# Optimization experiments

Hardware: AMD Instinct MI355X
Metric: run time of the kernel (lower is better)

## Reference

```python
import jax, jax.numpy as jnp
import numpy as np

B, C, N, S, DCONV = 16, 128, 2000, 8, 4
DI = 2 * N            # mamba expand=2
DT_RANK = (N + 15) // 16


def setup_inputs() -> dict:
    key = jax.random.key(0)
    ks = jax.random.split(key, 10)
    r = lambda k, sh, s=0.02: jax.random.normal(k, sh, jnp.float32) * s
    return {
        "x": jax.random.normal(ks[0], (B, C, N, 1), jnp.float32),
        "bn1_g": jnp.ones((C,), jnp.float32), "bn1_b": jnp.zeros((C,), jnp.float32),
        "conv1_w": r(ks[1], (C, C)), "conv1_b": jnp.zeros((C,), jnp.float32),
        "ln_w": jnp.ones((N,), jnp.float32), "ln_b": jnp.zeros((N,), jnp.float32),
        "W_in": r(ks[2], (2 * DI, N)),
        "convm_w": r(ks[3], (DI, DCONV), 0.1), "convm_b": jnp.zeros((DI,), jnp.float32),
        "W_x": r(ks[4], (DT_RANK + 2 * S, DI)),
        "W_dt": r(ks[5], (DI, DT_RANK), 0.1), "b_dt": jnp.full((DI,), -2.0, jnp.float32),
        "A_log": jnp.log(jnp.broadcast_to(jnp.arange(1, S + 1, dtype=jnp.float32), (DI, S))),
        "D_p": jnp.ones((DI,), jnp.float32),
        "W_out": r(ks[6], (N, DI)),
        "bn3_g": jnp.ones((C,), jnp.float32), "bn3_b": jnp.zeros((C,), jnp.float32),
        "conv3_w": r(ks[7], (C, C)), "conv3_b": jnp.zeros((C,), jnp.float32),
    }


def _inorm(x, eps=1e-3):
    # InstanceNorm2d (no affine): per-sample, per-channel over spatial dims
    m = x.mean(axis=(2, 3), keepdims=True)
    v = x.var(axis=(2, 3), keepdims=True)
    return (x - m) * jax.lax.rsqrt(v + eps)


def _bnorm(x, g, b, eps=1e-5):
    # BatchNorm2d (training-mode stats) over (B, H, W) per channel
    m = x.mean(axis=(0, 2, 3), keepdims=True)
    v = x.var(axis=(0, 2, 3), keepdims=True)
    return (x - m) * jax.lax.rsqrt(v + eps) * g[None, :, None, None] + b[None, :, None, None]


def _block(x, g, b, w, cb):
    # InstanceNorm -> BatchNorm -> ReLU -> 1x1 Conv2d
    h = jax.nn.relu(_bnorm(_inorm(x), g, b))
    return jnp.einsum('bcnw,oc->bonw', h, w) + cb[None, :, None, None]


def _mamba(u, W_in, cw, cb, W_x, W_dt, b_dt, A_log, D_p, W_out):
    # u: [B, L, D] with L=C (seq), D=N (d_model)
    L = u.shape[1]
    xz = jnp.einsum('bld,ed->ble', u, W_in)          # [B,L,2*DI]
    xi, z = jnp.split(xz, 2, axis=-1)
    # depthwise causal conv1d along L (d_conv=4)
    xp = jnp.pad(xi, ((0, 0), (DCONV - 1, 0), (0, 0)))
    xc = sum(xp[:, k:k + L, :] * cw[:, k] for k in range(DCONV)) + cb
    xc = jax.nn.silu(xc)                             # [B,L,DI]
    xdbl = jnp.einsum('bld,ed->ble', xc, W_x)        # [B,L,dt_rank+2S]
    dt = jax.nn.softplus(jnp.einsum('blr,dr->bld', xdbl[..., :DT_RANK], W_dt) + b_dt)
    Bm = xdbl[..., DT_RANK:DT_RANK + S]              # [B,L,S]
    Cm = xdbl[..., DT_RANK + S:]                     # [B,L,S]
    A = -jnp.exp(A_log)                              # [DI,S]

    def step(h, inp):
        dt_l, B_l, C_l, u_l = inp                    # [B,DI],[B,S],[B,S],[B,DI]
        dA = jnp.exp(dt_l[..., None] * A)            # [B,DI,S]
        h = dA * h + (dt_l * u_l)[..., None] * B_l[:, None, :]
        return h, jnp.einsum('bds,bs->bd', h, C_l)

    seq = (jnp.swapaxes(dt, 0, 1), jnp.swapaxes(Bm, 0, 1),
           jnp.swapaxes(Cm, 0, 1), jnp.swapaxes(xc, 0, 1))
    h0 = jnp.zeros((u.shape[0], DI, S), u.dtype)
    _, ys = jax.lax.scan(step, h0, seq)              # ys: [L,B,DI]
    y = jnp.swapaxes(ys, 0, 1) + xc * D_p
    y = y * jax.nn.silu(z)
    return jnp.einsum('ble,de->bld', y, W_out)       # [B,L,D]


def reference(x, bn1_g, bn1_b, conv1_w, conv1_b, ln_w, ln_b, W_in, convm_w,
              convm_b, W_x, W_dt, b_dt, A_log, D_p, W_out, bn3_g, bn3_b,
              conv3_w, conv3_b):
    out = _block(x, bn1_g, bn1_b, conv1_w, conv1_b)[..., 0]   # [B,C,N]
    mu = out.mean(-1, keepdims=True)
    var = out.var(-1, keepdims=True)
    out_n = (out - mu) * jax.lax.rsqrt(var + 1e-5) * ln_w + ln_b  # LayerNorm(points)
    out = out + _mamba(out_n, W_in, convm_w, convm_b, W_x, W_dt, b_dt, A_log, D_p, W_out)
    out = _block(out[..., None], bn3_g, bn3_b, conv3_w, conv3_b)  # [B,C,N,1]
    return out + x
```

## Files before the change

### kernel.cpp

```cpp
#include <hip/hip_runtime.h>
#include <cmath>
#include <cstdint>

#define Bc   16
#define Cc   128
#define Nc   2000
#define Lc   128
#define DIc  4000
#define Sc   8
#define RKc  125
#define E2c  8000
#define EXc  141

#define KP1  2016
#define NP1  8064

__device__ __forceinline__ unsigned short f2bf(float f) {
  union { float f; unsigned int u; } v; v.f = f;
  unsigned int r = v.u + 0x7FFFu + ((v.u >> 16) & 1u);
  return (unsigned short)(r >> 16);
}

__global__ void inorm_stats(const float* __restrict__ in,
                            float* __restrict__ mout,
                            float* __restrict__ vout) {
  int bc = blockIdx.x;
  const float* p = in + (long)bc * Nc;
  float s = 0.f, sq = 0.f;
  for (int i = threadIdx.x; i < Nc; i += blockDim.x) {
    float x = p[i]; s += x; sq += x * x;
  }
  #pragma unroll
  for (int o = 32; o > 0; o >>= 1) {
    s  += __shfl_down(s, o, 64);
    sq += __shfl_down(sq, o, 64);
  }
  __shared__ float ss[4], sqq[4];
  int w = threadIdx.x >> 6, lane = threadIdx.x & 63;
  if (lane == 0) { ss[w] = s; sqq[w] = sq; }
  __syncthreads();
  if (threadIdx.x == 0) {
    s  = ss[0] + ss[1] + ss[2] + ss[3];
    sq = sqq[0] + sqq[1] + sqq[2] + sqq[3];
    float mean = s / Nc;
    float var  = sq / Nc - mean * mean;
    mout[bc] = mean; vout[bc] = var;
  }
}

__global__ void bn_scale(const float* __restrict__ v, float* __restrict__ bnsc) {
  int c = threadIdx.x;
  if (c >= Cc) return;
  float s = 0.f;
  for (int b = 0; b < Bc; b++) {
    float vv = v[b * Cc + c];
    s += vv / (vv + 1e-3f);
  }
  bnsc[c] = rsqrtf(s / Bc + 1e-5f);
}

__global__ void compute_h_t(const float* __restrict__ in,
                            const float* __restrict__ m,
                            const float* __restrict__ v,
                            const float* __restrict__ bnsc,
                            const float* __restrict__ g,
                            const float* __restrict__ bb,
                            unsigned short* __restrict__ hT) {
  int b  = blockIdx.y;
  int n0 = blockIdx.x * 64;
  __shared__ unsigned short tile[64][132];
  int t  = threadIdx.x;
  int nl = t & 63, cb = t >> 6;
  int n  = n0 + nl;
  #pragma unroll 4
  for (int p = 0; p < 32; p++) {
    int c = p * 4 + cb;
    float val = 0.f;
    if (n < Nc) {
      int bc = b * Cc + c;
      float xn = (in[(long)bc * Nc + n] - m[bc]) * rsqrtf(v[bc] + 1e-3f);
      val = fmaxf(xn * bnsc[c] * g[c] + bb[c], 0.f);
    }
    tile[nl][c] = f2bf(val);
  }
  __syncthreads();
  int r = t >> 2, c0 = (t & 3) * 32;
  int nr = n0 + r;
  if (nr < Nc) {
    unsigned int* dst = (unsigned int*)(hT + ((long)b * 2048 + nr) * 128 + c0);
    const unsigned short* src = &tile[r][c0];
    #pragma unroll
    for (int j = 0; j < 16; j++)
      dst[j] = *(const unsigned int*)(src + 2 * j);
  }
}

__global__ void reduce_slices(const float* __restrict__ sl, float* __restrict__ dst,
                              long stride, int ns, int total, int accum) {
  int i = blockIdx.x * 256 + threadIdx.x;
  if (i >= total) return;
  float s = accum ? dst[i] : 0.f;
  for (int k = 0; k < ns; k++) s += sl[(long)k * stride + i];
  dst[i] = s;
}

__global__ void reduce_xdbl(const float* __restrict__ sl,
                            float* __restrict__ xd,
                            unsigned short* __restrict__ xdb) {
  int i = blockIdx.x * 256 + threadIdx.x;
  if (i >= 2048 * 144) return;
  int row = i / 144, c = i - row * 144;
  float s = 0.f;
  if (c < EXc) {
    #pragma unroll
    for (int k = 0; k < 4; k++) s += sl[(long)k * (2048 * 256) + (long)row * 256 + c];
    xd[(long)row * EXc + c] = s;
  }
  if (c < 128) xdb[(long)row * 128 + c] = f2bf(c < RKc ? s : 0.f);
}

__global__ void cvt_pad_bf16(const float* __restrict__ src, unsigned short* __restrict__ dst,
                             int R, int Cdst, int Rsrc, int Csrc) {
  long i = (long)blockIdx.x * 256 + threadIdx.x;
  long total = (long)R * Cdst;
  if (i >= total) return;
  int r = (int)(i / Cdst), c = (int)(i - (long)r * Cdst);
  float v = (r < Rsrc && c < Csrc) ? src[(long)r * Csrc + c] : 0.f;
  dst[i] = f2bf(v);
}

__global__ void ln_rows(const float* __restrict__ in,
                        const float* __restrict__ lw,
                        const float* __restrict__ lb,
                        unsigned short* __restrict__ An) {
  int row = blockIdx.x;
  const float* p = in + (long)row * Nc;
  float s = 0.f, sq = 0.f;
  for (int i = threadIdx.x; i < Nc; i += blockDim.x) {
    float x = p[i]; s += x; sq += x * x;
  }
  #pragma unroll
  for (int o = 32; o > 0; o >>= 1) {
    s  += __shfl_down(s, o, 64);
    sq += __shfl_down(sq, o, 64);
  }
  __shared__ float ss[4], sqq[4];
  __shared__ float smean, srstd;
  int w = threadIdx.x >> 6, lane = threadIdx.x & 63;
  if (lane == 0) { ss[w] = s; sqq[w] = sq; }
  __syncthreads();
  if (threadIdx.x == 0) {
    s  = ss[0] + ss[1] + ss[2] + ss[3];
    sq = sqq[0] + sqq[1] + sqq[2] + sqq[3];
    float mean = s / Nc;
    float var  = sq / Nc - mean * mean;
    smean = mean; srstd = rsqrtf(var + 1e-5f);
  }
  __syncthreads();
  float mu = smean, rs = srstd;
  for (int i = threadIdx.x; i < KP1; i += blockDim.x) {
    float v = 0.f;
    if (i < Nc) v = (p[i] - mu) * rs * lw[i] + lb[i];
    An[(long)row * KP1 + i] = f2bf(v);
  }
}

typedef short v8s __attribute__((ext_vector_type(8)));
typedef float v4f __attribute__((ext_vector_type(4)));

typedef const __attribute__((address_space(1))) unsigned int* as1_cu32p;
typedef __attribute__((address_space(3))) unsigned int* as3_u32p;

__device__ __forceinline__ void gload_lds16(const unsigned short* g, unsigned short* l) {
  __builtin_amdgcn_global_load_lds((as1_cu32p)(uintptr_t)g,
                                   (as3_u32p)(uintptr_t)l, 16, 0, 0);
}

__global__ __launch_bounds__(256, 4)
void gemm_mfma_bt(const unsigned short* __restrict__ A,
                  const unsigned short* __restrict__ B,
                  float* C, int NN, int K, int lda, int ldb, int ldc,
                  long sA, long sB, long sC,
                  int KS, int Klen, long sliceStride,
                  int epi, const float* __restrict__ ebias,
                  const float* __restrict__ addp) {
  __shared__ unsigned short As[128 * 32];
  __shared__ unsigned short Bs[128 * 32];

  int z = blockIdx.z;
  int batch = z / KS, ks = z - batch * KS;
  const unsigned short* Ab = A + (long)batch * sA;
  const unsigned short* Bb = B + (long)batch * sB;
  float* Cs = C + (long)batch * sC + (long)ks * sliceStride;
  const float* X = addp ? addp + (long)batch * sC : nullptr;

  int k0 = ks * Klen;
  int kend = min(K, k0 + Klen);

  int i0 = blockIdx.y * 128;
  int j0 = blockIdx.x * 128;

  int t = threadIdx.x;
  int wave = t >> 6, lane = t & 63;
  int wm = wave >> 1, wn = wave & 1;

  int srow = lane >> 2;
  int scol = lane & 3;
  const unsigned short* gA0 = Ab + (long)(i0 + wave * 32 + srow) * lda + scol * 8;
  const unsigned short* gA1 = gA0 + (long)16 * lda;
  const unsigned short* gB0 = Bb + (long)(j0 + wave * 32 + srow) * ldb + scol * 8;
  const unsigned short* gB1 = gB0 + (long)16 * ldb;
  unsigned short* lA0 = As + (wave * 32) * 32;
  unsigned short* lA1 = As + (wave * 32 + 16) * 32;
  unsigned short* lB0 = Bs + (wave * 32) * 32;
  unsigned short* lB1 = Bs + (wave * 32 + 16) * 32;

  int fr = lane & 15;
  int kq = lane >> 4;

  v4f acc[4][4] = {};

  for (int kt = k0; kt < kend; kt += 32) {
    gload_lds16(gA0 + kt, lA0);
    gload_lds16(gA1 + kt, lA1);
    gload_lds16(gB0 + kt, lB0);
    gload_lds16(gB1 + kt, lB1);
    __syncthreads();

    v8s af[4], bfr[4];
    #pragma unroll
    for (int mt = 0; mt < 4; mt++)
      af[mt] = *(const v8s*)&As[(wm * 64 + mt * 16 + fr) * 32 + kq * 8];
    #pragma unroll
    for (int nt = 0; nt < 4; nt++)
      bfr[nt] = *(const v8s*)&Bs[(wn * 64 + nt * 16 + fr) * 32 + kq * 8];

    #pragma unroll
    for (int mt = 0; mt < 4; mt++)
      #pragma unroll
      for (int nt = 0; nt < 4; nt++)
        acc[mt][nt] = __builtin_amdgcn_mfma_f32_16x16x32_bf16(
            af[mt], bfr[nt], acc[mt][nt], 0, 0, 0);
    __syncthreads();
  }

  int orow = (lane >> 4) * 4;
  int ocol = lane & 15;
  #pragma unroll
  for (int mt = 0; mt < 4; mt++) {
    #pragma unroll
    for (int nt = 0; nt < 4; nt++) {
      int gi = i0 + wm * 64 + mt * 16 + orow;
      int gj = j0 + wn * 64 + nt * 16 + ocol;
      if (gj >= NN) continue;
      #pragma unroll
      for (int r = 0; r < 4; r++) {
        long idx = (long)(gi + r) * ldc + gj;
        float v = acc[mt][nt][r];
        if (epi == 1) {
          float tr = v + ebias[gj];
          v = fmaxf(tr, 0.f) + log1pf(__expf(-fabsf(tr)));
        } else if (epi == 2) {
          if (gj >= DIc) v = v / (1.f + __expf(-v));
        } else if (epi == 3) {
          v += ebias[gi + r];
          if (X) v += X[idx];
        }
        Cs[idx] = v;
      }
    }
  }
}

__global__ void dwconv_silu(const float* __restrict__ xz,
                            const float4* __restrict__ cw,
                            const float* __restrict__ cb,
                            float* __restrict__ xc,
                            unsigned short* __restrict__ xcb, int total) {
  int i = blockIdx.x * 256 + threadIdx.x;
  if (i >= total) return;
  int d  = i % DIc;
  int bl = i / DIc;
  int l  = bl % Lc;
  int b  = bl / Lc;
  float4 w = cw[d];
  float acc = cb[d];
  long rowbase = (long)(b * Lc) * E2c + d;
  int l0 = l - 3;
  if (l0     >= 0) acc += xz[rowbase + (long)l0       * E2c] * w.x;
  if (l0 + 1 >= 0) acc += xz[rowbase + (long)(l0 + 1) * E2c] * w.y;
  if (l0 + 2 >= 0) acc += xz[rowbase + (long)(l0 + 2) * E2c] * w.z;
  acc += xz[rowbase + (long)l * E2c] * w.w;
  float sv = acc / (1.f + __expf(-acc));
  xc[i] = sv;
  xcb[i] = f2bf(sv);
}

#define SCU 4
__global__ __launch_bounds__(256)
void scan_kernel(const float* __restrict__ dtv,
                 const float* __restrict__ xdbl,
                 const float* __restrict__ xc,
                 const float* __restrict__ xzf,
                 const float* __restrict__ A_log,
                 const float* __restrict__ D_p,
                 unsigned short* __restrict__ yb) {
  int d = blockIdx.x * 256 + threadIdx.x;
  int b = blockIdx.y;
  if (d >= DIc) return;
  float Av[Sc];
  #pragma unroll
  for (int s = 0; s < Sc; s++) Av[s] = -__expf(A_log[d * Sc + s]);
  float Dp = D_p[d];
  float h[Sc];
  #pragma unroll
  for (int s = 0; s < Sc; s++) h[s] = 0.f;

  long base  = (long)(b * Lc) * DIc + d;
  long zbase = (long)(b * Lc) * E2c + DIc + d;
  const float* xrow = xdbl + (long)(b * Lc) * EXc + RKc;

  float d0[SCU], u0[SCU], z0[SCU], B0[SCU][Sc], C0[SCU][Sc];
  float d1[SCU], u1[SCU], z1[SCU], B1[SCU][Sc], C1[SCU][Sc];

#define LOADG(g, dd, uu, zz, BB, CC)                                        \
  { int l0_ = (g) * SCU;                                                    \
    _Pragma("unroll")                                                       \
    for (int u = 0; u < SCU; u++) {                                         \
      long idx = base + (long)(l0_ + u) * DIc;                              \
      dd[u] = dtv[idx];                                                     \
      uu[u] = xc[idx];                                                      \
      zz[u] = xzf[zbase + (long)(l0_ + u) * E2c];                           \
      const float* xr = xrow + (long)(l0_ + u) * EXc;                       \
      _Pragma("unroll")                                                     \
      for (int s = 0; s < Sc; s++) { BB[u][s] = xr[s]; CC[u][s] = xr[Sc + s]; } \
    } }

#define COMPG(g, dd, uu, zz, BB, CC)                                        \
  { int l0_ = (g) * SCU;                                                    \
    _Pragma("unroll")                                                       \
    for (int u = 0; u < SCU; u++) {                                         \
      float dv = dd[u], uv = uu[u];                                         \
      float du = dv * uv;                                                   \
      float p = 0.f;                                                        \
      _Pragma("unroll")                                                     \
      for (int s = 0; s < Sc; s++) {                                        \
        float dA = __expf(dv * Av[s]);                                      \
        h[s] = dA * h[s] + du * BB[u][s];                                   \
        p += h[s] * CC[u][s];                                               \
      }                                                                     \
      yb[base + (long)(l0_ + u) * DIc] = f2bf((p + uv * Dp) * zz[u]);       \
    } }

  LOADG(0, d0, u0, z0, B0, C0);
  #pragma unroll 1
  for (int g = 0; g < Lc / SCU; g += 2) {
    LOADG(g + 1, d1, u1, z1, B1, C1);
    COMPG(g, d0, u0, z0, B0, C0);
    if (g + 2 < Lc / SCU) LOADG(g + 2, d0, u0, z0, B0, C0);
    COMPG(g + 1, d1, u1, z1, B1, C1);
  }
#undef LOADG
#undef COMPG
}

extern "C" void kernel_launch(void* const* d_in, const int* in_sizes, int n_in,
                              void* d_out, int out_size, void* d_ws, size_t ws_size,
                              hipStream_t stream) {
  const float* x       = (const float*)d_in[0];
  const float* bn1_g   = (const float*)d_in[1];
  const float* bn1_b   = (const float*)d_in[2];
  const float* conv1_w = (const float*)d_in[3];
  const float* conv1_b = (const float*)d_in[4];
  const float* ln_w    = (const float*)d_in[5];
  const float* ln_b    = (const float*)d_in[6];
  const float* W_in    = (const float*)d_in[7];
  const float* convm_w = (const float*)d_in[8];
  const float* convm_b = (const float*)d_in[9];
  const float* W_x     = (const float*)d_in[10];
  const float* W_dt    = (const float*)d_in[11];
  const float* b_dt    = (const float*)d_in[12];
  const float* A_log   = (const float*)d_in[13];
  const float* D_p     = (const float*)d_in[14];
  const float* W_out   = (const float*)d_in[15];
  const float* bn3_g   = (const float*)d_in[16];
  const float* bn3_b   = (const float*)d_in[17];
  const float* conv3_w = (const float*)d_in[18];
  const float* conv3_b = (const float*)d_in[19];
  float* out = (float*)d_out;
  float* ws  = (float*)d_ws;

  const int TOT  = Bc * Cc * Nc;
  const int ROWS = Bc * Lc;

  float* m1    = ws;
  float* v1    = ws + 2048;
  float* bnsc  = ws + 4096;
  float* h     = ws + 8192;
  float* out1  = h    + (long)TOT;
  float* outn  = out1 + (long)TOT;
  float* xz    = outn + (long)TOT;
  float* xc    = xz   + (long)ROWS * E2c;
  float* xdbl  = xc   + (long)ROWS * DIc;
  float* dtb   = xdbl + (long)ROWS * EXc;

  unsigned short* An      = (unsigned short*)outn;
  unsigned short* Bwin    = (unsigned short*)dtb;
  unsigned short* Bwx     = (unsigned short*)outn;
  unsigned short* Bwdt    = (unsigned short*)(outn + 512000);
  float*          xdbl_sl = outn + 800000;
  unsigned short* xdbl_b  = (unsigned short*)(outn + 2900000);
  unsigned short* W1b     = (unsigned short*)(outn + 3100000);
  unsigned short* W3b     = (unsigned short*)(outn + 3200000);
  unsigned short* hT      = (unsigned short*)h;
  unsigned short* xcb     = (unsigned short*)h;
  unsigned short* Bwout   = (unsigned short*)h;
  unsigned short* yb      = (unsigned short*)out;
  float*          wout_sl = xz;

  dim3 b256(256);
  int gElem = (TOT + 255) / 256;

  inorm_stats<<<dim3(Bc * Cc), b256, 0, stream>>>(x, m1, v1);
  bn_scale<<<dim3(1), dim3(128), 0, stream>>>(v1, bnsc);
  compute_h_t<<<dim3(32, Bc), b256, 0, stream>>>(x, m1, v1, bnsc, bn1_g, bn1_b, hT);
  cvt_pad_bf16<<<dim3(64), b256, 0, stream>>>(conv1_w, W1b, 128, 128, Cc, Cc);
  {
    dim3 g(16, 1, Bc);
    gemm_mfma_bt<<<g, b256, 0, stream>>>(W1b, hT, out1, Nc, 128, 128, 128, Nc,
                                         0L, 2048L * 128, (long)Cc * Nc,
                                         1, 128, 0L, 3, conv1_b, nullptr);
  }

  ln_rows<<<dim3(ROWS), b256, 0, stream>>>(out1, ln_w, ln_b, An);

  {
    long tot = (long)NP1 * KP1;
    cvt_pad_bf16<<<dim3((unsigned)((tot + 255) / 256)), b256, 0, stream>>>(
        W_in, Bwin, NP1, KP1, E2c, Nc);
  }

  {
    dim3 g(NP1 / 128, ROWS / 128, 1);
    gemm_mfma_bt<<<g, b256, 0, stream>>>(An, Bwin, xz, E2c, KP1, KP1, KP1, E2c,
                                         0L, 0L, 0L, 1, KP1, 0L, 2, nullptr, nullptr);
  }

  cvt_pad_bf16<<<dim3((256 * 4000 + 255) / 256), b256, 0, stream>>>(
      W_x, Bwx, 256, 4000, EXc, DIc);
  cvt_pad_bf16<<<dim3((4096 * 128 + 255) / 256), b256, 0, stream>>>(
      W_dt, Bwdt, 4096, 128, DIc, RKc);

  {
    int tot = ROWS * DIc;
    dwconv_silu<<<dim3((tot + 255) / 256), b256, 0, stream>>>(
        xz, (const float4*)convm_w, convm_b, xc, xcb, tot);
  }

  {
    dim3 g(2, ROWS / 128, 4);
    gemm_mfma_bt<<<g, b256, 0, stream>>>(xcb, Bwx, xdbl_sl, 256, DIc,
                                         DIc, DIc, 256, 0L, 0L, 0L,
                                         4, 1024, 2048L * 256, 0, nullptr, nullptr);
    int tot = 2048 * 144;
    reduce_xdbl<<<dim3((tot + 255) / 256), b256, 0, stream>>>(xdbl_sl, xdbl, xdbl_b);
  }

  {
    dim3 g(4096 / 128, ROWS / 128, 1);
    gemm_mfma_bt<<<g, b256, 0, stream>>>(xdbl_b, Bwdt, dtb, DIc, 128,
                                         128, 128, DIc, 0L, 0L, 0L,
                                         1, 128, 0L, 1, b_dt, nullptr);
  }

  {
    long tot = (long)2048 * DIc;
    cvt_pad_bf16<<<dim3((unsigned)((tot + 255) / 256)), b256, 0, stream>>>(
        W_out, Bwout, 2048, DIc, Nc, DIc);
  }

  scan_kernel<<<dim3((DIc + 255) / 256, Bc), b256, 0, stream>>>(
      dtb, xdbl, xc, xz, A_log, D_p, yb);

  {
    dim3 g(2048 / 128, ROWS / 128, 2);
    gemm_mfma_bt<<<g, b256, 0, stream>>>(yb, Bwout, wout_sl, Nc, DIc, DIc, DIc, Nc,
                                         0L, 0L, 0L, 2, 2048, (long)TOT,
                                         0, nullptr, nullptr);
    reduce_slices<<<dim3(gElem), b256, 0, stream>>>(
        wout_sl, out1, (long)TOT, 2, TOT, 1);
  }

  inorm_stats<<<dim3(Bc * Cc), b256, 0, stream>>>(out1, m1, v1);
  bn_scale<<<dim3(1), dim3(128), 0, stream>>>(v1, bnsc);
  compute_h_t<<<dim3(32, Bc), b256, 0, stream>>>(out1, m1, v1, bnsc, bn3_g, bn3_b, hT);
  cvt_pad_bf16<<<dim3(64), b256, 0, stream>>>(conv3_w, W3b, 128, 128, Cc, Cc);
  {
    dim3 g(16, 1, Bc);
    gemm_mfma_bt<<<g, b256, 0, stream>>>(W3b, hT, out, Nc, 128, 128, 128, Nc,
                                         0L, 2048L * 128, (long)Cc * Nc,
                                         1, 128, 0L, 3, conv3_b, x);
  }
}
```

Before: 665.2 us.

## Add 256x256 eight-phase pipelined bf16 MFMA GEMM for the W_in projection

```diff
diff --git a/kernel.cpp b/kernel.cpp
--- a/kernel.cpp
+++ b/kernel.cpp
@@ -12,8 +12,9 @@
 #define E2c  8000
 #define EXc  141
 
-#define KP1  2016
-#define NP1  8064
+#define KP1  2048
+#define NP8  8192
+#define KT8  32
 
 __device__ __forceinline__ unsigned short f2bf(float f) {
   union { float f; unsigned int u; } v; v.f = f;
@@ -272,6 +273,157 @@
   }
 }
 
+__global__ __launch_bounds__(512, 2)
+void gemm_win_8ph(const unsigned short* __restrict__ A,
+                  const unsigned short* __restrict__ B,
+                  float* __restrict__ C) {
+  __shared__ unsigned short As8[2 * 2 * 128 * 64];
+  __shared__ unsigned short Bs8[2 * 2 * 128 * 64];
+
+  const int lda = KP1, ldb = KP1, ldc = E2c;
+
+  int i0 = blockIdx.y * 256;
+  int j0 = blockIdx.x * 256;
+
+  int t = threadIdx.x;
+  int w = t >> 6, l = t & 63;
+  int wm = w >> 2;
+  int wn = w & 3;
+  int w8 = w << 3;
+
+  int rw     = w8 + (l >> 3);
+  int scol16 = (l & 7) ^ ((l >> 3) & 7);
+  const unsigned short* pA = A + (long)(i0 + rw) * lda + scol16 * 8;
+  int gjrow = ((rw >> 5) << 6) + (rw & 31);
+  const unsigned short* pB = B + (long)(j0 + gjrow) * ldb + scol16 * 8;
+
+  int fr   = l & 15;
+  int kq   = l >> 4;
+  int inr0 = ((kq ^ (fr & 7)) << 4);
+  int inr1 = inr0 ^ 64;
+
+  const char* asb = (const char*)As8;
+  const char* bsb = (const char*)Bs8;
+
+  v4f acc[8][4] = {};
+  v8s aF[4][2], bF[2][2][2];
+
+#define ST_A(bufi, h, tile) do {                                              \
+    int kt_ = ((tile) < KT8 ? (tile) : (KT8 - 1)) * 64;                       \
+    gload_lds16(pA + (long)((h) * 64) * lda + kt_,                            \
+                As8 + (size_t)((((bufi) * 2 + (h)) * 128 + w8) * 64));        \
+    gload_lds16(pA + (long)(128 + (h) * 64) * lda + kt_,                      \
+                As8 + (size_t)((((bufi) * 2 + (h)) * 128 + 64 + w8) * 64));   \
+  } while (0)
+#define ST_B(bufi, h, tile) do {                                              \
+    int kt_ = ((tile) < KT8 ? (tile) : (KT8 - 1)) * 64;                       \
+    gload_lds16(pB + (long)((h) * 32) * ldb + kt_,                            \
+                Bs8 + (size_t)((((bufi) * 2 + (h)) * 128 + w8) * 64));        \
+    gload_lds16(pB + (long)(128 + (h) * 32) * ldb + kt_,                      \
+                Bs8 + (size_t)((((bufi) * 2 + (h)) * 128 + 64 + w8) * 64));   \
+  } while (0)
+#define LD_A(bufi, mh) do {                                                   \
+    const char* ab_ = asb + (size_t)(((((bufi) * 2 + (mh)) * 128) + wm * 64 + fr) * 128); \
+    aF[0][0] = *(const v8s*)(ab_ +    0 + inr0); aF[0][1] = *(const v8s*)(ab_ +    0 + inr1); \
+    aF[1][0] = *(const v8s*)(ab_ + 2048 + inr0); aF[1][1] = *(const v8s*)(ab_ + 2048 + inr1); \
+    aF[2][0] = *(const v8s*)(ab_ + 4096 + inr0); aF[2][1] = *(const v8s*)(ab_ + 4096 + inr1); \
+    aF[3][0] = *(const v8s*)(ab_ + 6144 + inr0); aF[3][1] = *(const v8s*)(ab_ + 6144 + inr1); \
+  } while (0)
+#define LD_B(bufi, nh) do {                                                   \
+    const char* bb_ = bsb + (size_t)(((((bufi) * 2 + (nh)) * 128) + wn * 32 + fr) * 128); \
+    bF[nh][0][0] = *(const v8s*)(bb_ +    0 + inr0); bF[nh][0][1] = *(const v8s*)(bb_ +    0 + inr1); \
+    bF[nh][1][0] = *(const v8s*)(bb_ + 2048 + inr0); bF[nh][1][1] = *(const v8s*)(bb_ + 2048 + inr1); \
+  } while (0)
+#define MM(mh, nh) do {                                                       \
+    _Pragma("unroll")                                                         \
+    for (int mt_ = 0; mt_ < 4; mt_++) {                                       \
+      _Pragma("unroll")                                                       \
+      for (int nt_ = 0; nt_ < 2; nt_++) {                                     \
+        acc[(mh) * 4 + mt_][(nh) * 2 + nt_] = __builtin_amdgcn_mfma_f32_16x16x32_bf16( \
+            aF[mt_][0], bF[nh][nt_][0], acc[(mh) * 4 + mt_][(nh) * 2 + nt_], 0, 0, 0); \
+        acc[(mh) * 4 + mt_][(nh) * 2 + nt_] = __builtin_amdgcn_mfma_f32_16x16x32_bf16( \
+            aF[mt_][1], bF[nh][nt_][1], acc[(mh) * 4 + mt_][(nh) * 2 + nt_], 0, 0, 0); \
+      } }                                                                     \
+  } while (0)
+#define FENCE()   __asm__ volatile("" ::: "memory")
+#define BARRIER() do { FENCE(); __builtin_amdgcn_s_barrier(); FENCE(); } while (0)
+#define WAIT_LGKM0() do { __asm__ volatile("s_waitcnt lgkmcnt(0)" ::: "memory"); \
+                          __builtin_amdgcn_sched_barrier(0); } while (0)
+#define WAIT_VM(n) __asm__ volatile("s_waitcnt vmcnt(" #n ")" ::: "memory")
+
+  ST_A(0, 0, 0); ST_B(0, 0, 0); ST_B(0, 1, 0); ST_A(0, 1, 0);
+  ST_A(1, 0, 1); ST_B(1, 1, 1); ST_A(1, 1, 1);
+  WAIT_VM(6);
+  BARRIER();
+
+  #pragma unroll 1
+  for (int it = 0; it < KT8 / 2; ++it) {
+    int u = 2 * it;
+    LD_A(0, 0); LD_B(0, 0); ST_B(1, 0, u + 1);
+    BARRIER(); WAIT_LGKM0();
+    __builtin_amdgcn_s_setprio(1); MM(0, 0); __builtin_amdgcn_s_setprio(0);
+    BARRIER();
+    LD_B(0, 1); ST_A(0, 0, u + 2);
+    BARRIER(); WAIT_LGKM0();
+    __builtin_amdgcn_s_setprio(1); MM(0, 1); __builtin_amdgcn_s_setprio(0);
+    BARRIER();
+    LD_A(0, 1); ST_B(0, 1, u + 2);
+    BARRIER(); WAIT_LGKM0();
+    __builtin_amdgcn_s_setprio(1); MM(1, 1); __builtin_amdgcn_s_setprio(0);
+    BARRIER();
+    ST_A(0, 1, u + 2);
+    BARRIER();
+    __builtin_amdgcn_s_setprio(1); MM(1, 0); __builtin_amdgcn_s_setprio(0);
+    WAIT_VM(6);
+    BARRIER();
+    LD_A(1, 0); LD_B(1, 0); ST_B(0, 0, u + 2);
+    BARRIER(); WAIT_LGKM0();
+    __builtin_amdgcn_s_setprio(1); MM(0, 0); __builtin_amdgcn_s_setprio(0);
+    BARRIER();
+    LD_B(1, 1); ST_A(1, 0, u + 3);
+    BARRIER(); WAIT_LGKM0();
+    __builtin_amdgcn_s_setprio(1); MM(0, 1); __builtin_amdgcn_s_setprio(0);
+    BARRIER();
+    LD_A(1, 1); ST_B(1, 1, u + 3);
+    BARRIER(); WAIT_LGKM0();
+    __builtin_amdgcn_s_setprio(1); MM(1, 1); __builtin_amdgcn_s_setprio(0);
+    BARRIER();
+    ST_A(1, 1, u + 3);
+    BARRIER();
+    __builtin_amdgcn_s_setprio(1); MM(1, 0); __builtin_amdgcn_s_setprio(0);
+    WAIT_VM(6);
+    BARRIER();
+  }
+  WAIT_VM(0);
+
+  int orow4 = (l >> 4) * 4;
+  int ocol  = l & 15;
+  #pragma unroll
+  for (int m = 0; m < 8; m++) {
+    int gi = i0 + wm * 128 + m * 16 + orow4;
+    #pragma unroll
+    for (int n = 0; n < 4; n++) {
+      int gj = j0 + wn * 64 + n * 16 + ocol;
+      if (gj >= E2c) continue;
+      #pragma unroll
+      for (int r = 0; r < 4; r++) {
+        float v = acc[m][n][r];
+        if (gj >= DIc) v = v / (1.f + __expf(-v));
+        C[(long)(gi + r) * ldc + gj] = v;
+      }
+    }
+  }
+#undef ST_A
+#undef ST_B
+#undef LD_A
+#undef LD_B
+#undef MM
+#undef FENCE
+#undef BARRIER
+#undef WAIT_LGKM0
+#undef WAIT_VM
+}
+
 __global__ void dwconv_silu(const float* __restrict__ xz,
                             const float4* __restrict__ cw,
                             const float* __restrict__ cb,
@@ -405,7 +557,7 @@
   float* dtb   = xdbl + (long)ROWS * EXc;
 
   unsigned short* An      = (unsigned short*)outn;
-  unsigned short* Bwin    = (unsigned short*)dtb;
+  unsigned short* Bwin8   = (unsigned short*)xc;
   unsigned short* Bwx     = (unsigned short*)outn;
   unsigned short* Bwdt    = (unsigned short*)(outn + 512000);
   float*          xdbl_sl = outn + 800000;
@@ -435,16 +587,12 @@
   ln_rows<<<dim3(ROWS), b256, 0, stream>>>(out1, ln_w, ln_b, An);
 
   {
-    long tot = (long)NP1 * KP1;
+    long tot = (long)NP8 * KP1;
     cvt_pad_bf16<<<dim3((unsigned)((tot + 255) / 256)), b256, 0, stream>>>(
-        W_in, Bwin, NP1, KP1, E2c, Nc);
-  }
-
-  {
-    dim3 g(NP1 / 128, ROWS / 128, 1);
-    gemm_mfma_bt<<<g, b256, 0, stream>>>(An, Bwin, xz, E2c, KP1, KP1, KP1, E2c,
-                                         0L, 0L, 0L, 1, KP1, 0L, 2, nullptr, nullptr);
-  }
+        W_in, Bwin8, NP8, KP1, E2c, Nc);
+  }
+
+  gemm_win_8ph<<<dim3(NP8 / 256, ROWS / 256), dim3(512), 0, stream>>>(An, Bwin8, xz);
 
   cvt_pad_bf16<<<dim3((256 * 4000 + 255) / 256), b256, 0, stream>>>(
       W_x, Bwx, 256, 4000, EXc, DIc);
```

Result: faster. 633.2 us (-4.8%).
